# Kernel tuning notes

Hardware: AMD Instinct MI355X
Metric: run time of the kernel (lower is better)

Reference implementation:

```python
import jax, jax.numpy as jnp
import numpy as np

EPS = 1e-5  # BatchNorm2d default eps


def conv1x1(x, w, b):
    # x: (B,C,H,W), w: (O,C), b: (O,)
    return jnp.einsum('bchw,oc->bohw', x, w) + b[None, :, None, None]


def bn_relu(x, g, beta, m, v):
    # inference-mode BatchNorm2d followed by ReLU; per-channel params (C,)
    s = g * jax.lax.rsqrt(v + EPS)
    return jax.nn.relu(x * s[None, :, None, None] + (beta - m * s)[None, :, None, None])


def setup_inputs() -> dict:
    key = jax.random.key(0)
    B, Cin, H, W = 4, 512, 64, 64
    Ck, Cv, Cout = 256, 256, 512
    ks = jax.random.split(key, 16)
    WSCALE = 0.03  # keep activations / softmax logits in a sane range

    def branch_params(k, first_in):
        k = jax.random.split(k, 8)
        return dict(
            w1=jax.random.normal(k[0], (Ck, first_in), jnp.float32) * WSCALE,
            b1=jax.random.normal(k[1], (Ck,), jnp.float32) * 0.01,
            g1=jnp.ones((Ck,), jnp.float32),
            beta1=jnp.zeros((Ck,), jnp.float32),
            m1=jax.random.normal(k[2], (Ck,), jnp.float32) * 0.05,
            v1=jax.random.uniform(k[3], (Ck,), jnp.float32, 0.5, 1.5),
            w2=jax.random.normal(k[4], (Ck, Ck), jnp.float32) * WSCALE,
            b2=jax.random.normal(k[5], (Ck,), jnp.float32) * 0.01,
            g2=jnp.ones((Ck,), jnp.float32),
            beta2=jnp.zeros((Ck,), jnp.float32),
            m2=jax.random.normal(k[6], (Ck,), jnp.float32) * 0.05,
            v2=jax.random.uniform(k[7], (Ck,), jnp.float32, 0.5, 1.5),
        )

    kb = branch_params(ks[1], Cin)
    qb = branch_params(ks[2], Cin)
    d = {'x': jax.random.normal(ks[0], (B, Cin, H, W), jnp.float32)}
    for name, p in (('k', kb), ('q', qb)):
        for pk, pv in p.items():
            d[f'{name}_{pk}'] = pv
    d['v_w'] = jax.random.normal(ks[3], (Cv, Cin), jnp.float32) * WSCALE
    d['v_b'] = jax.random.normal(ks[4], (Cv,), jnp.float32) * 0.01
    d['o_w'] = jax.random.normal(ks[5], (Cout, Cv), jnp.float32) * WSCALE
    d['o_b'] = jax.random.normal(ks[6], (Cout,), jnp.float32) * 0.01
    return d


def reference(x,
              k_w1, k_b1, k_g1, k_beta1, k_m1, k_v1,
              k_w2, k_b2, k_g2, k_beta2, k_m2, k_v2,
              q_w1, q_b1, q_g1, q_beta1, q_m1, q_v1,
              q_w2, q_b2, q_g2, q_beta2, q_m2, q_v2,
              v_w, v_b, o_w, o_b):
    B, C, H, W = x.shape
    Ck = k_w1.shape[0]
    Cv = v_w.shape[0]
    N = H * W

    def branch(w1, b1, g1, be1, m1, v1, w2, b2, g2, be2, m2, v2):
        h = bn_relu(conv1x1(x, w1, b1), g1, be1, m1, v1)
        return bn_relu(conv1x1(h, w2, b2), g2, be2, m2, v2)

    value = conv1x1(x, v_w, v_b).reshape(B, Cv, N)                       # (B,Cv,N)
    query = branch(q_w1, q_b1, q_g1, q_beta1, q_m1, q_v1,
                   q_w2, q_b2, q_g2, q_beta2, q_m2, q_v2).reshape(B, Ck, N)
    keyf = branch(k_w1, k_b1, k_g1, k_beta1, k_m1, k_v1,
                  k_w2, k_b2, k_g2, k_beta2, k_m2, k_v2).reshape(B, Ck, N)

    # sim_map[b,n,m] = <query[:,n], key[:,m]> * Ck^-0.5, softmax over m
    sim = jnp.einsum('bcn,bcm->bnm', query, keyf) * (Ck ** -0.5)         # (B,N,N)
    attn = jax.nn.softmax(sim, axis=-1)
    ctx = jnp.einsum('bnm,bcm->bcn', attn, value).reshape(B, Cv, H, W)   # (B,Cv,H,W)
    return conv1x1(ctx, o_w, o_b)                                        # (B,Cout,H,W)
```

## Files before the change

kernel.cpp:

```cpp
#include <hip/hip_runtime.h>
#include <hip/hip_bf16.h>

typedef unsigned short u16;
typedef __attribute__((ext_vector_type(8))) unsigned short u16x8;
typedef __attribute__((ext_vector_type(4))) unsigned short u16x4;
typedef __attribute__((ext_vector_type(4))) float f32x4;

#define MFMA16(a,b,c) __builtin_amdgcn_mfma_f32_16x16x32_bf16((a),(b),(c),0,0,0)
#define LOG2E 1.44269504f

static __device__ __forceinline__ float b2f(u16 b) {
  unsigned int u = ((unsigned int)b) << 16;
  float f;
  __builtin_memcpy(&f, &u, 4);
  return f;
}
static __device__ __forceinline__ u16 f2b(float x) {
  __hip_bfloat16 h = __float2bfloat16(x);
  u16 u;
  __builtin_memcpy(&u, &h, 2);
  return u;
}
static __device__ __forceinline__ u16x8 ld8(const u16* p) {
  u16x8 v;
  __builtin_memcpy(&v, p, 16);
  return v;
}
static __device__ __forceinline__ void st8(u16* p, u16x8 v) {
  __builtin_memcpy(p, &v, 16);
}
#define MEMFENCE() __asm__ __volatile__("" ::: "memory")
static __device__ __forceinline__ bool is_fp32(const unsigned int* probe) {
  return probe[0] == 0x3F800000u;
}

typedef __attribute__((address_space(1))) const void gas_void;
typedef __attribute__((address_space(3))) void las_void;
static __device__ __forceinline__ void gload16(const u16* g, u16* l) {
  __builtin_amdgcn_global_load_lds((gas_void*)g, (las_void*)l, 16, 0, 0);
}

static __device__ __forceinline__ uint3 xcd_swz() {
  unsigned nx = gridDim.x, ny = gridDim.y;
  unsigned nwg = nx * ny * gridDim.z;
  unsigned lin = (blockIdx.z * ny + blockIdx.y) * nx + blockIdx.x;
  unsigned wg = (lin & 7u) * (nwg >> 3) + (lin >> 3);
  uint3 r;
  r.x = wg % nx;
  unsigned t = wg / nx;
  r.y = t % ny;
  r.z = t / ny;
  return r;
}

struct ParamPack {
  const void* p[28];
  int sz[28];
  int off[28];
};
__global__ __launch_bounds__(256)
void convert_params(ParamPack pk, u16* __restrict__ dst,
                    const unsigned int* __restrict__ probe) {
  const int b = blockIdx.x;
  const int n = pk.sz[b], o = pk.off[b];
  if (is_fp32(probe)) {
    const float* s = (const float*)pk.p[b];
    for (int i = threadIdx.x; i < n; i += 256) dst[o + i] = f2b(s[i]);
  } else {
    const u16* s = (const u16*)pk.p[b];
    for (int i = threadIdx.x; i < n; i += 256) dst[o + i] = s[i];
  }
}

__global__ __launch_bounds__(256)
void transpose_cn(const void* __restrict__ xv, u16* __restrict__ xt,
                  const unsigned int* __restrict__ probe) {
  __shared__ u16 tile[64][65];
  const int b = blockIdx.z;
  const int n0 = blockIdx.x * 64, c0 = blockIdx.y * 64;
  const int tn = threadIdx.x & 63, tr = threadIdx.x >> 6;
  if (is_fp32(probe)) {
    const float* xb = (const float*)xv + (size_t)b * 512 * 4096;
    #pragma unroll
    for (int i = tr; i < 64; i += 4)
      tile[i][tn] = f2b(xb[(size_t)(c0 + i) * 4096 + n0 + tn]);
  } else {
    const u16* xb = (const u16*)xv + (size_t)b * 512 * 4096;
    #pragma unroll
    for (int i = tr; i < 64; i += 4)
      tile[i][tn] = xb[(size_t)(c0 + i) * 4096 + n0 + tn];
  }
  __syncthreads();
  u16* xtb = xt + (size_t)b * 4096 * 512;
  #pragma unroll
  for (int i = tr; i < 64; i += 4)
    xtb[(size_t)(n0 + i) * 512 + c0 + tn] = tile[tn][i];
}

static __device__ __forceinline__ void gemm_core(
    const u16* __restrict__ A, const u16* __restrict__ Bb, int K,
    int nb, int mb0, u16* __restrict__ lds, f32x4 acc[2][4])
{
  const int tid = threadIdx.x;
  const int lane = tid & 63, wave = tid >> 6;
  const int quad = lane >> 4, l15 = lane & 15;
  const int mb1 = mb0 + 64;

  const u16* a0 = A + (size_t)(mb0 + l15) * K + quad * 8;
  const u16* a1 = A + (size_t)(mb1 + l15) * K + quad * 8;

  const int srow = tid >> 3;
  const int scol = ((tid & 7) ^ (srow & 7)) * 8;
  const u16* bsrc = Bb + (size_t)(nb + srow) * K + scol;
  const int swz = (l15 & 7) * 8;

  #pragma unroll
  for (int i = 0; i < 2; ++i)
    #pragma unroll
    for (int t = 0; t < 4; ++t)
      acc[i][t] = (f32x4){0.f, 0.f, 0.f, 0.f};

  {
    u16* d = lds + wave * 512;
    gload16(bsrc, d);
    gload16(bsrc + (size_t)32 * K, d + 2048);
  }
  u16x8 afA0 = ld8(a0), afA1 = ld8(a0 + 32);
  u16x8 afB0 = ld8(a1), afB1 = ld8(a1 + 32);
  u16x8 anA0 = afA0, anA1 = afA1, anB0 = afB0, anB1 = afB1;

  int cur = 0;
  for (int k = 0; k < K; k += 64) {
    __syncthreads();
    if (k + 64 < K) {
      u16* d = lds + (cur ^ 1) * 4096 + wave * 512;
      gload16(bsrc + k + 64, d);
      gload16(bsrc + (size_t)32 * K + k + 64, d + 2048);
      anA0 = ld8(a0 + k + 64); anA1 = ld8(a0 + k + 96);
      anB0 = ld8(a1 + k + 64); anB1 = ld8(a1 + k + 96);
    }
    const u16* bl = lds + cur * 4096;
    #pragma unroll
    for (int t = 0; t < 4; ++t) {
      const u16* br = bl + (size_t)(t * 16 + l15) * 64;
      u16x8 bf0 = ld8(br + ((quad * 8) ^ swz));
      acc[0][t] = MFMA16(afA0, bf0, acc[0][t]);
      acc[1][t] = MFMA16(afB0, bf0, acc[1][t]);
      u16x8 bf1 = ld8(br + (((4 + quad) * 8) ^ swz));
      acc[0][t] = MFMA16(afA1, bf1, acc[0][t]);
      acc[1][t] = MFMA16(afB1, bf1, acc[1][t]);
    }
    afA0 = anA0; afA1 = anA1; afB0 = anB0; afB1 = anB1;
    cur ^= 1;
  }
}

static __device__ __forceinline__ void epi_bn_T(
    f32x4 acc[2][4], u16* __restrict__ ob, int M, int nb, int mb0,
    const u16* __restrict__ bias, const u16* __restrict__ g,
    const u16* __restrict__ be, const u16* __restrict__ mu,
    const u16* __restrict__ vr)
{
  const int lane = threadIdx.x & 63;
  const int quad = lane >> 4, l15 = lane & 15;
  #pragma unroll
  for (int i = 0; i < 2; ++i) {
    const int mb = mb0 + i * 64;
    float sc[4], sh[4];
    #pragma unroll
    for (int r = 0; r < 4; ++r) {
      int o = mb + quad * 4 + r;
      float s = b2f(g[o]) * rsqrtf(b2f(vr[o]) + 1e-5f);
      sc[r] = s;
      sh[r] = b2f(be[o]) - b2f(mu[o]) * s + b2f(bias[o]) * s;
    }
    #pragma unroll
    for (int t = 0; t < 4; ++t) {
      int n = nb + t * 16 + l15;
      float y0 = fmaxf(acc[i][t][0] * sc[0] + sh[0], 0.f);
      float y1 = fmaxf(acc[i][t][1] * sc[1] + sh[1], 0.f);
      float y2 = fmaxf(acc[i][t][2] * sc[2] + sh[2], 0.f);
      float y3 = fmaxf(acc[i][t][3] * sc[3] + sh[3], 0.f);
      u16x4 pk = { f2b(y0), f2b(y1), f2b(y2), f2b(y3) };
      __builtin_memcpy(&ob[(size_t)n * M + mb + quad * 4], &pk, 8);
    }
  }
}

static __device__ __forceinline__ void epi_plain_N(
    f32x4 acc[2][4], u16* __restrict__ ob, int nb, int mb0,
    const u16* __restrict__ bias)
{
  const int N = 4096;
  const int lane = threadIdx.x & 63;
  const int quad = lane >> 4, l15 = lane & 15;
  #pragma unroll
  for (int i = 0; i < 2; ++i) {
    const int mb = mb0 + i * 64;
    float sh[4];
    #pragma unroll
    for (int r = 0; r < 4; ++r) sh[r] = b2f(bias[mb + quad * 4 + r]);
    #pragma unroll
    for (int t = 0; t < 4; ++t) {
      int n = nb + t * 16 + l15;
      #pragma unroll
      for (int r = 0; r < 4; ++r)
        ob[(size_t)(mb + quad * 4 + r) * N + n] = f2b(acc[i][t][r] + sh[r]);
    }
  }
}

__global__ __launch_bounds__(256)
void gemm_f1(const u16* __restrict__ xt, u16* __restrict__ vv,
             u16* __restrict__ h1q, u16* __restrict__ h1k,
             const u16* __restrict__ vw, const u16* __restrict__ vb,
             const u16* __restrict__ qw, const u16* __restrict__ qb,
             const u16* __restrict__ qg, const u16* __restrict__ qbe,
             const u16* __restrict__ qm, const u16* __restrict__ qv,
             const u16* __restrict__ kw, const u16* __restrict__ kb,
             const u16* __restrict__ kg, const u16* __restrict__ kbe,
             const u16* __restrict__ km, const u16* __restrict__ kv)
{
  __shared__ u16 blds[2 * 64 * 64];
  const uint3 wg = xcd_swz();
  const int b = wg.z;
  const int sel = wg.y >> 1;
  const int wave = threadIdx.x >> 6;
  const int nb = wg.x * 64;
  const int mb0 = (wg.y & 1) * 128 + wave * 16;

  const u16* Bb = xt + (size_t)b * 4096 * 512;
  const u16* A = (sel == 0) ? vw : (sel == 1) ? qw : kw;

  f32x4 acc[2][4];
  gemm_core(A, Bb, 512, nb, mb0, blds, acc);

  if (sel == 0) {
    epi_plain_N(acc, vv + (size_t)b * 256 * 4096, nb, mb0, vb);
  } else if (sel == 1) {
    epi_bn_T(acc, h1q + (size_t)b * 4096 * 256, 256, nb, mb0,
             qb, qg, qbe, qm, qv);
  } else {
    epi_bn_T(acc, h1k + (size_t)b * 4096 * 256, 256, nb, mb0,
             kb, kg, kbe, km, kv);
  }
}

__global__ __launch_bounds__(256)
void gemm_f2(const u16* __restrict__ h1q, const u16* __restrict__ h1k,
             u16* __restrict__ qt, u16* __restrict__ kt,
             const u16* __restrict__ qw, const u16* __restrict__ qb,
             const u16* __restrict__ qg, const u16* __restrict__ qbe,
             const u16* __restrict__ qm, const u16* __restrict__ qv,
             const u16* __restrict__ kw, const u16* __restrict__ kb,
             const u16* __restrict__ kg, const u16* __restrict__ kbe,
             const u16* __restrict__ km, const u16* __restrict__ kv)
{
  __shared__ u16 blds[2 * 64 * 64];
  const uint3 wg = xcd_swz();
  const int b = wg.z >> 1;
  const int br = wg.z & 1;
  const int wave = threadIdx.x >> 6;
  const int nb = wg.x * 64;
  const int mb0 = wg.y * 128 + wave * 16;

  const u16* Bb = (br ? h1k : h1q) + (size_t)b * 4096 * 256;
  const u16* A = br ? kw : qw;

  f32x4 acc[2][4];
  gemm_core(A, Bb, 256, nb, mb0, blds, acc);

  u16* ob = (br ? kt : qt) + (size_t)b * 4096 * 256;
  if (br) epi_bn_T(acc, ob, 256, nb, mb0, kb, kg, kbe, km, kv);
  else    epi_bn_T(acc, ob, 256, nb, mb0, qb, qg, qbe, qm, qv);
}

__global__ __launch_bounds__(256)
void gemm_nt(const u16* __restrict__ A, const u16* __restrict__ Bt,
             void* __restrict__ outv, int M, int K,
             const u16* __restrict__ bias,
             const unsigned int* __restrict__ oprobe)
{
  const int N = 4096;
  __shared__ u16 blds[2 * 64 * 64];
  const uint3 wg = xcd_swz();
  const int b = wg.z;
  const int lane = threadIdx.x & 63, wave = threadIdx.x >> 6;
  const int quad = lane >> 4, l15 = lane & 15;
  const int nb = wg.x * 64;
  const int mb0 = wg.y * 128 + wave * 16;

  const u16* Bb = Bt + (size_t)b * N * K;
  f32x4 acc[2][4];
  gemm_core(A, Bb, K, nb, mb0, blds, acc);

  if (oprobe != nullptr && is_fp32(oprobe)) {
    float* ob = (float*)outv + (size_t)b * M * N;
    #pragma unroll
    for (int i = 0; i < 2; ++i) {
      const int mb = mb0 + i * 64;
      float sh[4];
      #pragma unroll
      for (int r = 0; r < 4; ++r) sh[r] = b2f(bias[mb + quad * 4 + r]);
      #pragma unroll
      for (int t = 0; t < 4; ++t) {
        int n = nb + t * 16 + l15;
        #pragma unroll
        for (int r = 0; r < 4; ++r)
          ob[(size_t)(mb + quad * 4 + r) * N + n] = acc[i][t][r] + sh[r];
      }
    }
  } else {
    u16* ob = (u16*)outv + (size_t)b * M * N;
    #pragma unroll
    for (int i = 0; i < 2; ++i) {
      const int mb = mb0 + i * 64;
      float sh[4];
      #pragma unroll
      for (int r = 0; r < 4; ++r) sh[r] = b2f(bias[mb + quad * 4 + r]);
      #pragma unroll
      for (int t = 0; t < 4; ++t) {
        int n = nb + t * 16 + l15;
        #pragma unroll
        for (int r = 0; r < 4; ++r)
          ob[(size_t)(mb + quad * 4 + r) * N + n] = f2b(acc[i][t][r] + sh[r]);
      }
    }
  }
}

__global__ __launch_bounds__(256, 2)
void attn_k5(const u16* __restrict__ Qt, const u16* __restrict__ Kt,
             const u16* __restrict__ V, u16* __restrict__ part,
             float* __restrict__ scales)
{
  const int N = 4096, D = 256, SPLIT = 2048;
  __shared__ u16 kt_lds[2][32][256];
  __shared__ u16 v_lds[2][256][32];
  __shared__ u16 p_lds[4][16][40];

  const uint3 wg = xcd_swz();
  const int b = wg.y;
  const int sp = wg.z;
  const int tid = threadIdx.x;
  const int lane = tid & 63, wave = tid >> 6;
  const int quad = lane >> 4, l15 = lane & 15;
  const int q0 = wg.x * 64 + wave * 16;
  const int k0 = sp * SPLIT;

  const u16* Qb = Qt + (size_t)b * N * D;
  const u16* Kb = Kt + (size_t)b * N * D;
  const u16* Vb = V + (size_t)b * D * N;

  const int krow = tid >> 5;
  const int kcol = ((tid & 31) ^ krow) * 8;
  const int vswz = (tid >> 3) & 7;

  auto stage = [&](int bi, int m0) {
    u16* kd = (bi ? &kt_lds[1][0][0] : &kt_lds[0][0][0]) + wave * 512;
    u16* vd = (bi ? &v_lds[1][0][0] : &v_lds[0][0][0]) + wave * 512;
    #pragma unroll
    for (int j = 0; j < 4; ++j) {
      gload16(Kb + (size_t)(m0 + j * 8 + krow) * D + kcol, kd + j * 2048);
      int gc = (j * 256 + tid) ^ vswz;
      gload16(Vb + (size_t)(gc >> 2) * N + m0 + (gc & 3) * 8, vd + j * 2048);
    }
  };

  u16x8 qf[8];
  #pragma unroll
  for (int ks = 0; ks < 8; ++ks)
    qf[ks] = ld8(&Qb[(size_t)(q0 + l15) * D + ks * 32 + quad * 8]);

  u16x8 ones;
  #pragma unroll
  for (int i = 0; i < 8; ++i) ones[i] = 0x3F80;

  f32x4 oacc[16];
  #pragma unroll
  for (int ct = 0; ct < 16; ++ct) oacc[ct] = (f32x4){0.f, 0.f, 0.f, 0.f};
  f32x4 lacc = (f32x4){0.f, 0.f, 0.f, 0.f};
  float mrow[4] = {-1e30f, -1e30f, -1e30f, -1e30f};

  stage(0, k0);
  int cur = 0;
  for (int it = 0; it < SPLIT / 32; ++it) {
    __syncthreads();
    if (it + 1 < SPLIT / 32) stage(cur ^ 1, k0 + (it + 1) * 32);

    const u16* kl = cur ? &kt_lds[1][0][0] : &kt_lds[0][0][0];
    const u16* vl = cur ? &v_lds[1][0][0] : &v_lds[0][0][0];

    f32x4 s0 = (f32x4){0.f, 0.f, 0.f, 0.f};
    f32x4 s1 = (f32x4){0.f, 0.f, 0.f, 0.f};
    __builtin_amdgcn_s_setprio(1);
    #pragma unroll
    for (int ks = 0; ks < 8; ++ks) {
      int c0 = ((ks * 4 + quad) * 8) ^ ((l15 & 7) * 8);
      u16x8 bk0 = ld8(kl + (size_t)l15 * 256 + c0);
      u16x8 bk1 = ld8(kl + (size_t)(16 + l15) * 256 + c0);
      s0 = MFMA16(qf[ks], bk0, s0);
      s1 = MFMA16(qf[ks], bk1, s1);
    }
    __builtin_amdgcn_s_setprio(0);

    float adiff[4];
    int chg = 0;
    #pragma unroll
    for (int r = 0; r < 4; ++r) {
      float a = s0[r] * 0.0625f;
      float c = s1[r] * 0.0625f;
      float mx = fmaxf(a, c);
      mx = fmaxf(mx, __shfl_xor(mx, 1));
      mx = fmaxf(mx, __shfl_xor(mx, 2));
      mx = fmaxf(mx, __shfl_xor(mx, 4));
      mx = fmaxf(mx, __shfl_xor(mx, 8));
      float mnew = fmaxf(mrow[r], mx);
      adiff[r] = mrow[r] - mnew;
      chg |= (mnew > mrow[r]) ? 1 : 0;
      mrow[r] = mnew;
      float p0 = exp2f((a - mnew) * LOG2E);
      float p1 = exp2f((c - mnew) * LOG2E);
      p_lds[wave][quad * 4 + r][l15] = f2b(p0);
      p_lds[wave][quad * 4 + r][16 + l15] = f2b(p1);
    }
    if (__any(chg)) {
      float alpha[4];
      #pragma unroll
      for (int r = 0; r < 4; ++r) alpha[r] = exp2f(adiff[r] * LOG2E);
      #pragma unroll
      for (int ct = 0; ct < 16; ++ct) {
        oacc[ct][0] *= alpha[0];
        oacc[ct][1] *= alpha[1];
        oacc[ct][2] *= alpha[2];
        oacc[ct][3] *= alpha[3];
      }
      lacc[0] *= alpha[0];
      lacc[1] *= alpha[1];
      lacc[2] *= alpha[2];
      lacc[3] *= alpha[3];
    }
    MEMFENCE();

    u16x8 pf = ld8(&p_lds[wave][l15][quad * 8]);

    __builtin_amdgcn_s_setprio(1);
    #pragma unroll
    for (int ct = 0; ct < 16; ++ct) {
      int gc = ct * 64 + l15 * 4 + quad;
      u16x8 vf = ld8(vl + (size_t)(gc ^ (l15 >> 1)) * 8);
      oacc[ct] = MFMA16(pf, vf, oacc[ct]);
    }
    lacc = MFMA16(pf, ones, lacc);
    __builtin_amdgcn_s_setprio(0);
    MEMFENCE();
    cur ^= 1;
  }

  float inv[4];
  #pragma unroll
  for (int r = 0; r < 4; ++r) inv[r] = 1.f / lacc[r];
  u16* Pb = part + (size_t)sp * 4194304 + (size_t)b * N * D;
  #pragma unroll
  for (int ct = 0; ct < 16; ++ct) {
    #pragma unroll
    for (int r = 0; r < 4; ++r) {
      Pb[(size_t)(q0 + quad * 4 + r) * D + ct * 16 + l15] =
          f2b(oacc[ct][r] * inv[r]);
    }
  }
  if (l15 == 0) {
    #pragma unroll
    for (int r = 0; r < 4; ++r) {
      size_t row = (size_t)q0 + quad * 4 + r;
      size_t o = (((size_t)sp * 4 + b) * 4096 + row) * 2;
      scales[o + 0] = mrow[r];
      scales[o + 1] = lacc[r];
    }
  }
}

__global__ __launch_bounds__(256)
void attn_merge(u16* __restrict__ part, const float* __restrict__ scales) {
  const int n = blockIdx.x, b = blockIdx.y, c = threadIdx.x;
  const size_t stride = (size_t)4194304;
  const size_t row = ((size_t)b * 4096 + n) * 256;
  const size_t s0 = (((size_t)0 * 4 + b) * 4096 + n) * 2;
  const size_t s1 = (((size_t)1 * 4 + b) * 4096 + n) * 2;
  float m0 = scales[s0], l0 = scales[s0 + 1];
  float m1 = scales[s1], l1 = scales[s1 + 1];
  float m = fmaxf(m0, m1);
  float w0 = exp2f((m0 - m) * LOG2E) * l0;
  float w1 = exp2f((m1 - m) * LOG2E) * l1;
  float inv = 1.f / (w0 + w1);
  w0 *= inv; w1 *= inv;
  float v = b2f(part[row + c]) * w0 + b2f(part[stride + row + c]) * w1;
  part[row + c] = f2b(v);
}

extern "C" void kernel_launch(void* const* d_in, const int* in_sizes, int n_in,
                              void* d_out, int out_size, void* d_ws, size_t ws_size,
                              hipStream_t stream) {
  (void)n_in; (void)out_size;
  if (ws_size < (size_t)43789824) return;

  const unsigned int* probe = (const unsigned int*)d_in[3];

  ParamPack pk;
  int off = 0;
  for (int i = 0; i < 28; ++i) {
    pk.p[i] = d_in[i + 1];
    pk.sz[i] = in_sizes[i + 1];
    pk.off[i] = off;
    off += in_sizes[i + 1];
  }

  u16* ws  = (u16*)d_ws;
  u16* xt  = ws;
  u16* h1q = ws + 8388608;
  u16* h1k = ws + 12582912;
  u16* vv  = ws + 16777216;
  u16* qt  = ws;
  u16* kt  = ws + 4194304;
  u16* part = ws + 8388608;
  u16* ot  = part;
  u16* P   = ws + 20971520;
  float* scales = (float*)(ws + 21632768);

  const u16 *ck_w1 = P + pk.off[0],  *ck_b1 = P + pk.off[1],
            *ck_g1 = P + pk.off[2],  *ck_be1 = P + pk.off[3],
            *ck_m1 = P + pk.off[4],  *ck_v1 = P + pk.off[5],
            *ck_w2 = P + pk.off[6],  *ck_b2 = P + pk.off[7],
            *ck_g2 = P + pk.off[8],  *ck_be2 = P + pk.off[9],
            *ck_m2 = P + pk.off[10], *ck_v2 = P + pk.off[11],
            *cq_w1 = P + pk.off[12], *cq_b1 = P + pk.off[13],
            *cq_g1 = P + pk.off[14], *cq_be1 = P + pk.off[15],
            *cq_m1 = P + pk.off[16], *cq_v1 = P + pk.off[17],
            *cq_w2 = P + pk.off[18], *cq_b2 = P + pk.off[19],
            *cq_g2 = P + pk.off[20], *cq_be2 = P + pk.off[21],
            *cq_m2 = P + pk.off[22], *cq_v2 = P + pk.off[23],
            *cv_w  = P + pk.off[24], *cv_b  = P + pk.off[25],
            *co_w  = P + pk.off[26], *co_b  = P + pk.off[27];

  convert_params<<<28, 256, 0, stream>>>(pk, P, probe);
  transpose_cn<<<dim3(64, 8, 4), 256, 0, stream>>>(d_in[0], xt, probe);

  gemm_f1<<<dim3(64, 6, 4), 256, 0, stream>>>(xt, vv, h1q, h1k,
      cv_w, cv_b,
      cq_w1, cq_b1, cq_g1, cq_be1, cq_m1, cq_v1,
      ck_w1, ck_b1, ck_g1, ck_be1, ck_m1, ck_v1);
  gemm_f2<<<dim3(64, 2, 8), 256, 0, stream>>>(h1q, h1k, qt, kt,
      cq_w2, cq_b2, cq_g2, cq_be2, cq_m2, cq_v2,
      ck_w2, ck_b2, ck_g2, ck_be2, ck_m2, ck_v2);
  attn_k5<<<dim3(64, 4, 2), 256, 0, stream>>>(qt, kt, vv, part, scales);
  attn_merge<<<dim3(4096, 4), 256, 0, stream>>>(part, scales);
  gemm_nt<<<dim3(64, 4, 4), 256, 0, stream>>>(co_w, ot, d_out, 512, 256,
      co_b, probe);
}
```

Before: 416.1 us.

## Lazy softmax max rescaling in attention and vectorize param convert and merge

The attention inner loop now skips the per-tile cross-lane max reduction and accumulator rescale unless a new score exceeds the running max by more than a threshold, so it uses a stale max most of the time. Separately, parameter conversion uses 4- and 8-wide vector loads and stores, and the split merge kernel processes four rows per block with 4-element vector accesses. The lazy max trades shuffles and rescale work for possibly larger exponent values, which stay bounded by the threshold of 8 in log space. Exact softmax is still recovered through the final normalization by the accumulated row sum.

After: 353.8 us. 1.18x faster.

```diff
diff --git a/kernel.cpp b/kernel.cpp
--- a/kernel.cpp
+++ b/kernel.cpp
@@ -65,10 +65,17 @@
   const int n = pk.sz[b], o = pk.off[b];
   if (is_fp32(probe)) {
     const float* s = (const float*)pk.p[b];
-    for (int i = threadIdx.x; i < n; i += 256) dst[o + i] = f2b(s[i]);
+    for (int i = threadIdx.x * 4; i + 3 < n; i += 1024) {
+      float4 v;
+      __builtin_memcpy(&v, s + i, 16);
+      u16x4 w = { f2b(v.x), f2b(v.y), f2b(v.z), f2b(v.w) };
+      __builtin_memcpy(dst + o + i, &w, 8);
+    }
+    for (int t = (n & ~3) + threadIdx.x; t < n; t += 256) dst[o + t] = f2b(s[t]);
   } else {
     const u16* s = (const u16*)pk.p[b];
-    for (int i = threadIdx.x; i < n; i += 256) dst[o + i] = s[i];
+    for (int i = threadIdx.x * 8; i + 7 < n; i += 2048) st8(dst + o + i, ld8(s + i));
+    for (int t = (n & ~7) + threadIdx.x; t < n; t += 256) dst[o + t] = s[t];
   }
 }
 
@@ -404,30 +411,27 @@
     }
     __builtin_amdgcn_s_setprio(0);
 
-    float adiff[4];
-    int chg = 0;
+    float a[4], c[4];
+    int bad = 0;
     #pragma unroll
     for (int r = 0; r < 4; ++r) {
-      float a = s0[r] * 0.0625f;
-      float c = s1[r] * 0.0625f;
-      float mx = fmaxf(a, c);
-      mx = fmaxf(mx, __shfl_xor(mx, 1));
-      mx = fmaxf(mx, __shfl_xor(mx, 2));
-      mx = fmaxf(mx, __shfl_xor(mx, 4));
-      mx = fmaxf(mx, __shfl_xor(mx, 8));
-      float mnew = fmaxf(mrow[r], mx);
-      adiff[r] = mrow[r] - mnew;
-      chg |= (mnew > mrow[r]) ? 1 : 0;
-      mrow[r] = mnew;
-      float p0 = exp2f((a - mnew) * LOG2E);
-      float p1 = exp2f((c - mnew) * LOG2E);
-      p_lds[wave][quad * 4 + r][l15] = f2b(p0);
-      p_lds[wave][quad * 4 + r][16 + l15] = f2b(p1);
-    }
-    if (__any(chg)) {
+      a[r] = s0[r] * 0.0625f;
+      c[r] = s1[r] * 0.0625f;
+      bad |= (fmaxf(a[r], c[r]) - mrow[r] > 8.f) ? 1 : 0;
+    }
+    if (__builtin_expect(__any(bad), 0)) {
       float alpha[4];
       #pragma unroll
-      for (int r = 0; r < 4; ++r) alpha[r] = exp2f(adiff[r] * LOG2E);
+      for (int r = 0; r < 4; ++r) {
+        float mx = fmaxf(a[r], c[r]);
+        mx = fmaxf(mx, __shfl_xor(mx, 1));
+        mx = fmaxf(mx, __shfl_xor(mx, 2));
+        mx = fmaxf(mx, __shfl_xor(mx, 4));
+        mx = fmaxf(mx, __shfl_xor(mx, 8));
+        float mnew = fmaxf(mrow[r], mx);
+        alpha[r] = exp2f((mrow[r] - mnew) * LOG2E);
+        mrow[r] = mnew;
+      }
       #pragma unroll
       for (int ct = 0; ct < 16; ++ct) {
         oacc[ct][0] *= alpha[0];
@@ -440,6 +444,13 @@
       lacc[2] *= alpha[2];
       lacc[3] *= alpha[3];
     }
+    #pragma unroll
+    for (int r = 0; r < 4; ++r) {
+      float p0 = exp2f((a[r] - mrow[r]) * LOG2E);
+      float p1 = exp2f((c[r] - mrow[r]) * LOG2E);
+      p_lds[wave][quad * 4 + r][l15] = f2b(p0);
+      p_lds[wave][quad * 4 + r][16 + l15] = f2b(p1);
+    }
     MEMFENCE();
 
     u16x8 pf = ld8(&p_lds[wave][l15][quad * 8]);
@@ -482,7 +493,9 @@
 
 __global__ __launch_bounds__(256)
 void attn_merge(u16* __restrict__ part, const float* __restrict__ scales) {
-  const int n = blockIdx.x, b = blockIdx.y, c = threadIdx.x;
+  const int b = blockIdx.y;
+  const int n = blockIdx.x * 4 + (threadIdx.x >> 6);
+  const int c = (threadIdx.x & 63) * 4;
   const size_t stride = (size_t)4194304;
   const size_t row = ((size_t)b * 4096 + n) * 256;
   const size_t s0 = (((size_t)0 * 4 + b) * 4096 + n) * 2;
@@ -494,8 +507,14 @@
   float w1 = exp2f((m1 - m) * LOG2E) * l1;
   float inv = 1.f / (w0 + w1);
   w0 *= inv; w1 *= inv;
-  float v = b2f(part[row + c]) * w0 + b2f(part[stride + row + c]) * w1;
-  part[row + c] = f2b(v);
+  u16x4 p0, p1;
+  __builtin_memcpy(&p0, &part[row + c], 8);
+  __builtin_memcpy(&p1, &part[stride + row + c], 8);
+  u16x4 o;
+  #pragma unroll
+  for (int i = 0; i < 4; ++i)
+    o[i] = f2b(b2f(p0[i]) * w0 + b2f(p1[i]) * w1);
+  __builtin_memcpy(&part[row + c], &o, 8);
 }
 
 extern "C" void kernel_launch(void* const* d_in, const int* in_sizes, int n_in,
@@ -553,7 +572,7 @@
       cq_w2, cq_b2, cq_g2, cq_be2, cq_m2, cq_v2,
       ck_w2, ck_b2, ck_g2, ck_be2, ck_m2, ck_v2);
   attn_k5<<<dim3(64, 4, 2), 256, 0, stream>>>(qt, kt, vv, part, scales);
-  attn_merge<<<dim3(4096, 4), 256, 0, stream>>>(part, scales);
+  attn_merge<<<dim3(1024, 4), 256, 0, stream>>>(part, scales);
   gemm_nt<<<dim3(64, 4, 4), 256, 0, stream>>>(co_w, ot, d_out, 512, 256,
       co_b, probe);
 }
```
